# Performance work log

Hardware: AMD Instinct MI355X
Metric: run time of the kernel (lower is better)

The kernel has to match this reference:

```python
import jax, jax.numpy as jnp
import numpy as np
from math import factorial

ZETA = [1, 2, 3, 4]          # configs['zeta']=4 -> range(1,5)
NZETA = len(ZETA)
NRAD = 16
NLAMBDA = 2
NAT = 4000
NEDGE = 100000
ZMAX = max(ZETA)


def _make_lxlylz(zmax):
    tr, fn = [], []
    for s in range(zmax + 1):
        for lx in range(s + 1):
            for ly in range(s - lx + 1):
                lz = s - lx - ly
                tr.append((lx, ly, lz))
                fn.append(factorial(s) / (factorial(lx) * factorial(ly) * factorial(lz)))
    return np.asarray(tr, np.int32), np.asarray(fn, np.float32)


def setup_inputs() -> dict:
    key = jax.random.key(0)
    k1, k2, k3, k4 = jax.random.split(key, 4)
    rij = jax.random.normal(k1, (NEDGE, 3), dtype=jnp.float32)
    rij_unit = rij / jnp.linalg.norm(rij, axis=-1, keepdims=True)
    radial_ij = jax.random.uniform(k2, (NEDGE, NRAD, NZETA + 1), dtype=jnp.float32)
    lambda_weights = jax.random.normal(k3, (NLAMBDA,), dtype=jnp.float32)
    first_atom_idx = jnp.sort(jax.random.randint(k4, (NEDGE,), 0, NAT, dtype=jnp.int32))
    tr, fn = _make_lxlylz(ZMAX)
    return {
        "rij_unit": rij_unit,
        "radial_ij": radial_ij,
        "lambda_weights": lambda_weights,
        "fact_norm": jnp.asarray(fn),
        "first_atom_idx": first_atom_idx,
        "lxlylz": jnp.asarray(tr),
        "lxlylz_sum": jnp.asarray(tr.sum(axis=-1).astype(np.int32)),
        "nat": NAT,
    }


def reference(rij_unit, radial_ij, lambda_weights, fact_norm,
              first_atom_idx, lxlylz, lxlylz_sum, nat):
    # angular monomials g_ij_lxlylz : [E, L]
    lf = lxlylz.astype(jnp.float32)
    g_ij = jnp.prod(rij_unit[:, None, :] ** lf[None, :, :], axis=-1) * fact_norm[None, :]
    # lambda^(lx+ly+lz) : [n_lambda, L]
    lam = lambda_weights[:, None] ** lxlylz_sum.astype(jnp.float32)[None, :]
    # two-body radial descriptor: segment-sum of last radial channel -> [nat, Nrad]
    radial_i = jax.ops.segment_sum(radial_ij[:, :, -1], first_atom_idx, num_segments=nat)
    feats = [radial_i]
    for r_idx, z in enumerate(ZETA):
        # gather-compute: [E, Nrad, L]
        g = jnp.einsum('ej,ek->ejk', radial_ij[:, :, r_idx], g_ij)
        # scatter-reduce over neighbors of each central atom -> [nat, Nrad, L]
        g_i = jax.ops.segment_sum(g, first_atom_idx, num_segments=nat)
        # three-body power contraction with lambda weights, norm 2^(1-z)
        gi3 = jnp.einsum('njk,lk->njl', g_i * g_i, lam) * jnp.float32(2.0 ** (1.0 - z))
        feats.append(gi3.reshape(nat, -1))
    return jnp.concatenate(feats, axis=-1)  # [nat, Nrad*(1 + n_lambda*nzeta)]
```

## Files before the change

kernel.cpp:

```cpp
#include <hip/hip_runtime.h>

#define NRAD 16
#define NCH  5
#define NZ   4
#define NMON 35
#define OUTW 144

__global__ __launch_bounds__(256) void mbp_kernel(
    const float* __restrict__ rij_unit,
    const float* __restrict__ radial_ij,
    const float* __restrict__ lambda_w,
    const float* __restrict__ fact_norm,
    const int*   __restrict__ first_atom,
    float* __restrict__ out,
    int E)
{
    const int n    = blockIdx.x;
    const int tid  = threadIdx.x;
    const int lane = tid & 63;
    const int sg   = tid >> 6;
    const int zi   = lane >> 4;
    const int r    = lane & 15;

    int lo = 0, hi = E;
    while (lo < hi) { int mid = (lo + hi) >> 1; if (first_atom[mid] < n) lo = mid + 1; else hi = mid; }
    const int start = lo;
    hi = E;
    while (lo < hi) { int mid = (lo + hi) >> 1; if (first_atom[mid] < n + 1) lo = mid + 1; else hi = mid; }
    const int end = lo;

    float acc[NMON];
    #pragma unroll
    for (int l = 0; l < NMON; ++l) acc[l] = 0.f;
    float acc2 = 0.f;

    for (int e = start + sg; e < end; e += 4) {
        const float x = rij_unit[e * 3 + 0];
        const float y = rij_unit[e * 3 + 1];
        const float z = rij_unit[e * 3 + 2];
        const float rad = radial_ij[(e * NRAD + r) * NCH + zi];
        if (zi == 0) acc2 += radial_ij[(e * NRAD + r) * NCH + 4];

        const float x2 = x * x, x3 = x2 * x, x4 = x2 * x2;
        const float y2 = y * y, y3 = y2 * y, y4 = y2 * y2;
        const float z2 = z * z, z3 = z2 * z, z4 = z2 * z2;
        const float xy = x * y, xz = x * z, yz = y * z;

        acc[0]  += rad;
        acc[1]  = fmaf(rad, z,       acc[1]);
        acc[2]  = fmaf(rad, y,       acc[2]);
        acc[3]  = fmaf(rad, x,       acc[3]);
        acc[4]  = fmaf(rad, z2,      acc[4]);
        acc[5]  = fmaf(rad, yz,      acc[5]);
        acc[6]  = fmaf(rad, y2,      acc[6]);
        acc[7]  = fmaf(rad, xz,      acc[7]);
        acc[8]  = fmaf(rad, xy,      acc[8]);
        acc[9]  = fmaf(rad, x2,      acc[9]);
        acc[10] = fmaf(rad, z3,      acc[10]);
        acc[11] = fmaf(rad, y * z2,  acc[11]);
        acc[12] = fmaf(rad, y2 * z,  acc[12]);
        acc[13] = fmaf(rad, y3,      acc[13]);
        acc[14] = fmaf(rad, x * z2,  acc[14]);
        acc[15] = fmaf(rad, xy * z,  acc[15]);
        acc[16] = fmaf(rad, x * y2,  acc[16]);
        acc[17] = fmaf(rad, x2 * z,  acc[17]);
        acc[18] = fmaf(rad, x2 * y,  acc[18]);
        acc[19] = fmaf(rad, x3,      acc[19]);
        acc[20] = fmaf(rad, z4,      acc[20]);
        acc[21] = fmaf(rad, y * z3,  acc[21]);
        acc[22] = fmaf(rad, y2 * z2, acc[22]);
        acc[23] = fmaf(rad, y3 * z,  acc[23]);
        acc[24] = fmaf(rad, y4,      acc[24]);
        acc[25] = fmaf(rad, x * z3,  acc[25]);
        acc[26] = fmaf(rad, xy * z2, acc[26]);
        acc[27] = fmaf(rad, x * y2 * z, acc[27]);
        acc[28] = fmaf(rad, x * y3,  acc[28]);
        acc[29] = fmaf(rad, x2 * z2, acc[29]);
        acc[30] = fmaf(rad, x2 * yz, acc[30]);
        acc[31] = fmaf(rad, x2 * y2, acc[31]);
        acc[32] = fmaf(rad, x3 * z,  acc[32]);
        acc[33] = fmaf(rad, x3 * y,  acc[33]);
        acc[34] = fmaf(rad, x4,      acc[34]);
    }

    __shared__ float red[NMON + 1][256];
    #pragma unroll
    for (int l = 0; l < NMON; ++l) red[l][tid] = acc[l];
    red[NMON][tid] = acc2;
    __syncthreads();

    if (tid < 64) {
        float a[NMON];
        #pragma unroll
        for (int l = 0; l < NMON; ++l)
            a[l] = (red[l][tid] + red[l][tid + 64]) + (red[l][tid + 128] + red[l][tid + 192]);
        const float a2 = (red[NMON][tid] + red[NMON][tid + 64]) +
                         (red[NMON][tid + 128] + red[NMON][tid + 192]);

        const float l0 = lambda_w[0], l1 = lambda_w[1];
        const float p0[5] = {1.f, l0, l0 * l0, l0 * l0 * l0, (l0 * l0) * (l0 * l0)};
        const float p1[5] = {1.f, l1, l1 * l1, l1 * l1 * l1, (l1 * l1) * (l1 * l1)};
        const int lsum_tab[NMON] = {0, 1,1,1, 2,2,2,2,2,2,
                                    3,3,3,3,3,3,3,3,3,3,
                                    4,4,4,4,4,4,4,4,4,4,4,4,4,4,4};
        float s0 = 0.f, s1 = 0.f;
        #pragma unroll
        for (int l = 0; l < NMON; ++l) {
            const float f = fact_norm[l];
            const float v = a[l] * f;
            const float v2 = v * v;
            s0 = fmaf(v2, p0[lsum_tab[l]], s0);
            s1 = fmaf(v2, p1[lsum_tab[l]], s1);
        }
        const float scale = 1.0f / (float)(1 << zi);
        float* orow = out + (long)n * OUTW;
        orow[16 + zi * 32 + r * 2 + 0] = s0 * scale;
        orow[16 + zi * 32 + r * 2 + 1] = s1 * scale;
        if (zi == 0) orow[r] = a2;
    }
}

extern "C" void kernel_launch(void* const* d_in, const int* in_sizes, int n_in,
                              void* d_out, int out_size, void* d_ws, size_t ws_size,
                              hipStream_t stream) {
    const float* rij_unit   = (const float*)d_in[0];
    const float* radial_ij  = (const float*)d_in[1];
    const float* lambda_w   = (const float*)d_in[2];
    const float* fact_norm  = (const float*)d_in[3];
    const int*   first_atom = (const int*)d_in[4];
    const int E   = in_sizes[4];
    const int nat = out_size / OUTW;

    mbp_kernel<<<nat, 256, 0, stream>>>(rij_unit, radial_ij, lambda_w, fact_norm,
                                        first_atom, (float*)d_out, E);
}
```

Before: 127.0 us.

## Precompute segment offsets and map one wave per atom without LDS reduction

Adds a small pre-kernel that builds CSR-style segment offsets from the sorted atom indices, replacing the two per-block binary searches. The main kernel now assigns one 64-lane wave per atom instead of a 256-thread block, which removes the shared-memory cross-wave reduction and the __syncthreads. The edge loop is unrolled by four to batch the loads. In exchange there is an extra kernel launch, and each wave walks its atom's ~25 edges serially, so there is less parallelism per atom. The acc2 accumulation now runs in every lane, but only the zi==0 lanes write it out.

Measured after the change: 107.7 us. -15.2%, faster.

```diff
diff --git a/kernel.cpp b/kernel.cpp
--- a/kernel.cpp
+++ b/kernel.cpp
@@ -2,122 +2,145 @@
 
 #define NRAD 16
 #define NCH  5
-#define NZ   4
 #define NMON 35
 #define OUTW 144
 
-__global__ __launch_bounds__(256) void mbp_kernel(
+__global__ __launch_bounds__(256) void seg_offsets(
+    const int* __restrict__ idx, int* __restrict__ seg, int E, int nat)
+{
+    int e = blockIdx.x * blockDim.x + threadIdx.x;
+    if (e >= E) return;
+    if (e == 0) {
+        const int b = idx[0];
+        for (int n = 0; n <= b; ++n) seg[n] = 0;
+    } else {
+        const int a = idx[e - 1], b = idx[e];
+        for (int n = a + 1; n <= b; ++n) seg[n] = e;
+    }
+    if (e == E - 1) {
+        const int a = idx[E - 1];
+        for (int n = a + 1; n <= nat; ++n) seg[n] = E;
+    }
+}
+
+__device__ __forceinline__ void edge_body(
+    float x, float y, float z, float rad, float c4,
+    float acc[NMON], float& acc2)
+{
+    const float x2 = x * x, x3 = x2 * x, x4 = x2 * x2;
+    const float y2 = y * y, y3 = y2 * y, y4 = y2 * y2;
+    const float z2 = z * z, z3 = z2 * z, z4 = z2 * z2;
+    const float xy = x * y, xz = x * z, yz = y * z;
+
+    acc2 += c4;
+    acc[0]  += rad;
+    acc[1]  = fmaf(rad, z,        acc[1]);
+    acc[2]  = fmaf(rad, y,        acc[2]);
+    acc[3]  = fmaf(rad, x,        acc[3]);
+    acc[4]  = fmaf(rad, z2,       acc[4]);
+    acc[5]  = fmaf(rad, yz,       acc[5]);
+    acc[6]  = fmaf(rad, y2,       acc[6]);
+    acc[7]  = fmaf(rad, xz,       acc[7]);
+    acc[8]  = fmaf(rad, xy,       acc[8]);
+    acc[9]  = fmaf(rad, x2,       acc[9]);
+    acc[10] = fmaf(rad, z3,       acc[10]);
+    acc[11] = fmaf(rad, y * z2,   acc[11]);
+    acc[12] = fmaf(rad, y2 * z,   acc[12]);
+    acc[13] = fmaf(rad, y3,       acc[13]);
+    acc[14] = fmaf(rad, x * z2,   acc[14]);
+    acc[15] = fmaf(rad, xy * z,   acc[15]);
+    acc[16] = fmaf(rad, x * y2,   acc[16]);
+    acc[17] = fmaf(rad, x2 * z,   acc[17]);
+    acc[18] = fmaf(rad, x2 * y,   acc[18]);
+    acc[19] = fmaf(rad, x3,       acc[19]);
+    acc[20] = fmaf(rad, z4,       acc[20]);
+    acc[21] = fmaf(rad, y * z3,   acc[21]);
+    acc[22] = fmaf(rad, y2 * z2,  acc[22]);
+    acc[23] = fmaf(rad, y3 * z,   acc[23]);
+    acc[24] = fmaf(rad, y4,       acc[24]);
+    acc[25] = fmaf(rad, x * z3,   acc[25]);
+    acc[26] = fmaf(rad, xy * z2,  acc[26]);
+    acc[27] = fmaf(rad, x * y2 * z, acc[27]);
+    acc[28] = fmaf(rad, x * y3,   acc[28]);
+    acc[29] = fmaf(rad, x2 * z2,  acc[29]);
+    acc[30] = fmaf(rad, x2 * yz,  acc[30]);
+    acc[31] = fmaf(rad, x2 * y2,  acc[31]);
+    acc[32] = fmaf(rad, x3 * z,   acc[32]);
+    acc[33] = fmaf(rad, x3 * y,   acc[33]);
+    acc[34] = fmaf(rad, x4,       acc[34]);
+}
+
+__global__ __launch_bounds__(256) void mbp_main(
     const float* __restrict__ rij_unit,
     const float* __restrict__ radial_ij,
     const float* __restrict__ lambda_w,
     const float* __restrict__ fact_norm,
-    const int*   __restrict__ first_atom,
+    const int*   __restrict__ seg,
     float* __restrict__ out,
-    int E)
+    int nat)
 {
-    const int n    = blockIdx.x;
-    const int tid  = threadIdx.x;
-    const int lane = tid & 63;
-    const int sg   = tid >> 6;
-    const int zi   = lane >> 4;
-    const int r    = lane & 15;
+    const int wave = threadIdx.x >> 6;
+    const int n = blockIdx.x * 4 + wave;
+    if (n >= nat) return;
+    const int lane = threadIdx.x & 63;
+    const int zi = lane >> 4;
+    const int r  = lane & 15;
 
-    int lo = 0, hi = E;
-    while (lo < hi) { int mid = (lo + hi) >> 1; if (first_atom[mid] < n) lo = mid + 1; else hi = mid; }
-    const int start = lo;
-    hi = E;
-    while (lo < hi) { int mid = (lo + hi) >> 1; if (first_atom[mid] < n + 1) lo = mid + 1; else hi = mid; }
-    const int end = lo;
+    const int start = seg[n];
+    const int end   = seg[n + 1];
 
     float acc[NMON];
     #pragma unroll
     for (int l = 0; l < NMON; ++l) acc[l] = 0.f;
     float acc2 = 0.f;
 
-    for (int e = start + sg; e < end; e += 4) {
+    const int roff = r * NCH + zi;
+    const int coff = r * NCH + 4;
+
+    int e = start;
+    for (; e + 4 <= end; e += 4) {
+        float xs[4], ys[4], zs[4], rd[4], c4[4];
+        #pragma unroll
+        for (int u = 0; u < 4; ++u) {
+            const int ee = e + u;
+            xs[u] = rij_unit[ee * 3 + 0];
+            ys[u] = rij_unit[ee * 3 + 1];
+            zs[u] = rij_unit[ee * 3 + 2];
+            rd[u] = radial_ij[ee * (NRAD * NCH) + roff];
+            c4[u] = radial_ij[ee * (NRAD * NCH) + coff];
+        }
+        #pragma unroll
+        for (int u = 0; u < 4; ++u)
+            edge_body(xs[u], ys[u], zs[u], rd[u], c4[u], acc, acc2);
+    }
+    for (; e < end; ++e) {
         const float x = rij_unit[e * 3 + 0];
         const float y = rij_unit[e * 3 + 1];
         const float z = rij_unit[e * 3 + 2];
-        const float rad = radial_ij[(e * NRAD + r) * NCH + zi];
-        if (zi == 0) acc2 += radial_ij[(e * NRAD + r) * NCH + 4];
-
-        const float x2 = x * x, x3 = x2 * x, x4 = x2 * x2;
-        const float y2 = y * y, y3 = y2 * y, y4 = y2 * y2;
-        const float z2 = z * z, z3 = z2 * z, z4 = z2 * z2;
-        const float xy = x * y, xz = x * z, yz = y * z;
-
-        acc[0]  += rad;
-        acc[1]  = fmaf(rad, z,       acc[1]);
-        acc[2]  = fmaf(rad, y,       acc[2]);
-        acc[3]  = fmaf(rad, x,       acc[3]);
-        acc[4]  = fmaf(rad, z2,      acc[4]);
-        acc[5]  = fmaf(rad, yz,      acc[5]);
-        acc[6]  = fmaf(rad, y2,      acc[6]);
-        acc[7]  = fmaf(rad, xz,      acc[7]);
-        acc[8]  = fmaf(rad, xy,      acc[8]);
-        acc[9]  = fmaf(rad, x2,      acc[9]);
-        acc[10] = fmaf(rad, z3,      acc[10]);
-        acc[11] = fmaf(rad, y * z2,  acc[11]);
-        acc[12] = fmaf(rad, y2 * z,  acc[12]);
-        acc[13] = fmaf(rad, y3,      acc[13]);
-        acc[14] = fmaf(rad, x * z2,  acc[14]);
-        acc[15] = fmaf(rad, xy * z,  acc[15]);
-        acc[16] = fmaf(rad, x * y2,  acc[16]);
-        acc[17] = fmaf(rad, x2 * z,  acc[17]);
-        acc[18] = fmaf(rad, x2 * y,  acc[18]);
-        acc[19] = fmaf(rad, x3,      acc[19]);
-        acc[20] = fmaf(rad, z4,      acc[20]);
-        acc[21] = fmaf(rad, y * z3,  acc[21]);
-        acc[22] = fmaf(rad, y2 * z2, acc[22]);
-        acc[23] = fmaf(rad, y3 * z,  acc[23]);
-        acc[24] = fmaf(rad, y4,      acc[24]);
-        acc[25] = fmaf(rad, x * z3,  acc[25]);
-        acc[26] = fmaf(rad, xy * z2, acc[26]);
-        acc[27] = fmaf(rad, x * y2 * z, acc[27]);
-        acc[28] = fmaf(rad, x * y3,  acc[28]);
-        acc[29] = fmaf(rad, x2 * z2, acc[29]);
-        acc[30] = fmaf(rad, x2 * yz, acc[30]);
-        acc[31] = fmaf(rad, x2 * y2, acc[31]);
-        acc[32] = fmaf(rad, x3 * z,  acc[32]);
-        acc[33] = fmaf(rad, x3 * y,  acc[33]);
-        acc[34] = fmaf(rad, x4,      acc[34]);
+        const float rad = radial_ij[e * (NRAD * NCH) + roff];
+        const float c4v = radial_ij[e * (NRAD * NCH) + coff];
+        edge_body(x, y, z, rad, c4v, acc, acc2);
     }
 
-    __shared__ float red[NMON + 1][256];
+    const float l0 = lambda_w[0], l1 = lambda_w[1];
+    const float p0[5] = {1.f, l0, l0 * l0, l0 * l0 * l0, (l0 * l0) * (l0 * l0)};
+    const float p1[5] = {1.f, l1, l1 * l1, l1 * l1 * l1, (l1 * l1) * (l1 * l1)};
+    const int lsum_tab[NMON] = {0, 1,1,1, 2,2,2,2,2,2,
+                                3,3,3,3,3,3,3,3,3,3,
+                                4,4,4,4,4,4,4,4,4,4,4,4,4,4,4};
+    float s0 = 0.f, s1 = 0.f;
     #pragma unroll
-    for (int l = 0; l < NMON; ++l) red[l][tid] = acc[l];
-    red[NMON][tid] = acc2;
-    __syncthreads();
-
-    if (tid < 64) {
-        float a[NMON];
-        #pragma unroll
-        for (int l = 0; l < NMON; ++l)
-            a[l] = (red[l][tid] + red[l][tid + 64]) + (red[l][tid + 128] + red[l][tid + 192]);
-        const float a2 = (red[NMON][tid] + red[NMON][tid + 64]) +
-                         (red[NMON][tid + 128] + red[NMON][tid + 192]);
-
-        const float l0 = lambda_w[0], l1 = lambda_w[1];
-        const float p0[5] = {1.f, l0, l0 * l0, l0 * l0 * l0, (l0 * l0) * (l0 * l0)};
-        const float p1[5] = {1.f, l1, l1 * l1, l1 * l1 * l1, (l1 * l1) * (l1 * l1)};
-        const int lsum_tab[NMON] = {0, 1,1,1, 2,2,2,2,2,2,
-                                    3,3,3,3,3,3,3,3,3,3,
-                                    4,4,4,4,4,4,4,4,4,4,4,4,4,4,4};
-        float s0 = 0.f, s1 = 0.f;
-        #pragma unroll
-        for (int l = 0; l < NMON; ++l) {
-            const float f = fact_norm[l];
-            const float v = a[l] * f;
-            const float v2 = v * v;
-            s0 = fmaf(v2, p0[lsum_tab[l]], s0);
-            s1 = fmaf(v2, p1[lsum_tab[l]], s1);
-        }
-        const float scale = 1.0f / (float)(1 << zi);
-        float* orow = out + (long)n * OUTW;
-        orow[16 + zi * 32 + r * 2 + 0] = s0 * scale;
-        orow[16 + zi * 32 + r * 2 + 1] = s1 * scale;
-        if (zi == 0) orow[r] = a2;
+    for (int l = 0; l < NMON; ++l) {
+        const float v = acc[l] * fact_norm[l];
+        const float v2 = v * v;
+        s0 = fmaf(v2, p0[lsum_tab[l]], s0);
+        s1 = fmaf(v2, p1[lsum_tab[l]], s1);
     }
+    const float scale = 1.0f / (float)(1 << zi);
+    float* orow = out + (long)n * OUTW;
+    orow[16 + zi * 32 + r * 2 + 0] = s0 * scale;
+    orow[16 + zi * 32 + r * 2 + 1] = s1 * scale;
+    if (zi == 0) orow[r] = acc2;
 }
 
 extern "C" void kernel_launch(void* const* d_in, const int* in_sizes, int n_in,
@@ -131,6 +154,9 @@
     const int E   = in_sizes[4];
     const int nat = out_size / OUTW;
 
-    mbp_kernel<<<nat, 256, 0, stream>>>(rij_unit, radial_ij, lambda_w, fact_norm,
-                                        first_atom, (float*)d_out, E);
+    int* seg = (int*)d_ws;
+
+    seg_offsets<<<(E + 255) / 256, 256, 0, stream>>>(first_atom, seg, E, nat);
+    mbp_main<<<(nat + 3) / 4, 256, 0, stream>>>(rij_unit, radial_ij, lambda_w,
+                                                fact_norm, seg, (float*)d_out, nat);
 }
```
